# Optimization experiments

Measured on AMD Instinct MI355X. Metric: run time of the kernel, lower is better.

Reference implementation:

```python
import jax, jax.numpy as jnp
import numpy as np

EPS = 1e-8
N = 4
B = 1_000_000


def setup_inputs() -> dict:
    key = jax.random.key(0)
    g = jax.random.normal(key, (B, N, N), dtype=jnp.float32)
    # SPD covariance-like matrices: G G^T + 0.1 I (well-conditioned, distinct eigvals)
    x = jnp.einsum('bik,bjk->bij', g, g) / N + 0.1 * jnp.eye(N, dtype=jnp.float32)
    return {"x": x}


def reference(x):
    # 1) symmetrize + epsilon regularization (ensure SPD)
    sym = 0.5 * (x + jnp.swapaxes(x, -1, -2)) + EPS * jnp.eye(N, dtype=x.dtype)
    # 2) exact matrix log via eigendecomposition
    w, v = jnp.linalg.eigh(sym)                      # w: [B, N], v: [B, N, N]
    log_w = jnp.log(jnp.maximum(w, EPS))
    logm = jnp.einsum('bik,bk,bjk->bij', v, log_w, v)  # V diag(log w) V^T
    # 3) re-symmetrize
    logm = 0.5 * (logm + jnp.swapaxes(logm, -1, -2))
    # 4) upper-triangular vectorization, row-major (i, j>=i) order
    iu, ju = jnp.triu_indices(N)
    return logm[:, iu, ju]                           # [B, N*(N+1)//2]
```

## Files before the change

### kernel.cpp

```cpp
#include <hip/hip_runtime.h>
#include <math.h>

#ifndef NSWEEP
#define NSWEEP 5
#endif

#define EPSV 1e-8f

__device__ __forceinline__ float fast_sqrtf(float x) {
#if __has_builtin(__builtin_amdgcn_sqrtf)
  return __builtin_amdgcn_sqrtf(x);
#else
  return sqrtf(x);
#endif
}
__device__ __forceinline__ float fast_rcpf(float x) {
#if __has_builtin(__builtin_amdgcn_rcpf)
  return __builtin_amdgcn_rcpf(x);
#else
  return 1.0f / x;
#endif
}
__device__ __forceinline__ float fast_rsqf(float x) {
#if __has_builtin(__builtin_amdgcn_rsqf)
  return __builtin_amdgcn_rsqf(x);
#else
  return rsqrtf(x);
#endif
}
__device__ __forceinline__ float fast_logf(float x) {
#if __has_builtin(__builtin_amdgcn_logf)
  return __builtin_amdgcn_logf(x) * 0.6931471805599453f;
#else
  return logf(x);
#endif
}

#define JROT(APP, AQQ, APQ, AK1P, AK1Q, AK2P, AK2Q,                       \
             VP0, VQ0, VP1, VQ1, VP2, VQ2, VP3, VQ3)                      \
  do {                                                                    \
    float a_ = APQ;                                                       \
    float d_ = AQQ - APP;                                                 \
    float a2_ = a_ + a_;                                                  \
    float r_ = fast_sqrtf(fmaf(d_, d_, a2_ * a2_));                       \
    float den_ = fmaxf(fabsf(d_) + r_, 1e-30f);                          \
                        \
    float num_ = __int_as_float(__float_as_int(a2_) ^                     \
                                (__float_as_int(d_) & 0x80000000));       \
    float t_ = num_ * fast_rcpf(den_);                                    \
    float c_ = fast_rsqf(fmaf(t_, t_, 1.0f));                             \
    float s_ = t_ * c_;                                                   \
    float ta_ = t_ * a_;                                                  \
    APP = APP - ta_;                                                      \
    AQQ = AQQ + ta_;                                                      \
    APQ = 0.0f;                                                           \
    {                                                                     \
      float kp_ = AK1P, kq_ = AK1Q;                                       \
      AK1P = fmaf(c_, kp_, -s_ * kq_);                                    \
      AK1Q = fmaf(s_, kp_, c_ * kq_);                                     \
    }                                                                     \
    {                                                                     \
      float kp_ = AK2P, kq_ = AK2Q;                                       \
      AK2P = fmaf(c_, kp_, -s_ * kq_);                                    \
      AK2Q = fmaf(s_, kp_, c_ * kq_);                                     \
    }                                                                     \
    {                                                                     \
      float p_ = VP0, q_ = VQ0;                                           \
      VP0 = fmaf(c_, p_, -s_ * q_);                                       \
      VQ0 = fmaf(s_, p_, c_ * q_);                                        \
    }                                                                     \
    {                                                                     \
      float p_ = VP1, q_ = VQ1;                                           \
      VP1 = fmaf(c_, p_, -s_ * q_);                                       \
      VQ1 = fmaf(s_, p_, c_ * q_);                                        \
    }                                                                     \
    {                                                                     \
      float p_ = VP2, q_ = VQ2;                                           \
      VP2 = fmaf(c_, p_, -s_ * q_);                                       \
      VQ2 = fmaf(s_, p_, c_ * q_);                                        \
    }                                                                     \
    {                                                                     \
      float p_ = VP3, q_ = VQ3;                                           \
      VP3 = fmaf(c_, p_, -s_ * q_);                                       \
      VQ3 = fmaf(s_, p_, c_ * q_);                                        \
    }                                                                     \
  } while (0)

__global__ __launch_bounds__(256) void TangentSpaceLayer_64141041598486_kernel(
    const float* __restrict__ x, float* __restrict__ out, int B) {
  __shared__ __align__(16) float so[256 * 10];
  const int t = threadIdx.x;
  const int m = blockIdx.x * 256 + t;

  if (m < B) {
    const float* p = x + (size_t)m * 16;
    float4 r0 = *(const float4*)(p + 0);
    float4 r1 = *(const float4*)(p + 4);
    float4 r2 = *(const float4*)(p + 8);
    float4 r3 = *(const float4*)(p + 12);

    float a00 = r0.x + EPSV;
    float a01 = 0.5f * (r0.y + r1.x);
    float a02 = 0.5f * (r0.z + r2.x);
    float a03 = 0.5f * (r0.w + r3.x);
    float a11 = r1.y + EPSV;
    float a12 = 0.5f * (r1.z + r2.y);
    float a13 = 0.5f * (r1.w + r3.y);
    float a22 = r2.z + EPSV;
    float a23 = 0.5f * (r2.w + r3.z);
    float a33 = r3.w + EPSV;

    float v00 = 1.f, v01 = 0.f, v02 = 0.f, v03 = 0.f;
    float v10 = 0.f, v11 = 1.f, v12 = 0.f, v13 = 0.f;
    float v20 = 0.f, v21 = 0.f, v22 = 1.f, v23 = 0.f;
    float v30 = 0.f, v31 = 0.f, v32 = 0.f, v33 = 1.f;

#pragma unroll 1
    for (int sweep = 0; sweep < NSWEEP; ++sweep) {
      JROT(a00, a11, a01, a02, a12, a03, a13,
           v00, v01, v10, v11, v20, v21, v30, v31);
      JROT(a00, a22, a02, a01, a12, a03, a23,
           v00, v02, v10, v12, v20, v22, v30, v32);
      JROT(a00, a33, a03, a01, a13, a02, a23,
           v00, v03, v10, v13, v20, v23, v30, v33);
      JROT(a11, a22, a12, a01, a02, a13, a23,
           v01, v02, v11, v12, v21, v22, v31, v32);
      JROT(a11, a33, a13, a01, a03, a12, a23,
           v01, v03, v11, v13, v21, v23, v31, v33);
      JROT(a22, a33, a23, a02, a03, a12, a13,
           v02, v03, v12, v13, v22, v23, v32, v33);
    }

    float lw0 = fast_logf(fmaxf(a00, EPSV));
    float lw1 = fast_logf(fmaxf(a11, EPSV));
    float lw2 = fast_logf(fmaxf(a22, EPSV));
    float lw3 = fast_logf(fmaxf(a33, EPSV));

    float w00 = v00 * lw0, w01 = v01 * lw1, w02 = v02 * lw2, w03 = v03 * lw3;
    float w10 = v10 * lw0, w11 = v11 * lw1, w12 = v12 * lw2, w13 = v13 * lw3;
    float w20 = v20 * lw0, w21 = v21 * lw1, w22 = v22 * lw2, w23 = v23 * lw3;
    float w30 = v30 * lw0, w31 = v31 * lw1, w32 = v32 * lw2, w33 = v33 * lw3;

    float* sp = so + t * 10;
    sp[0] = fmaf(w00, v00, fmaf(w01, v01, fmaf(w02, v02, w03 * v03)));
    sp[1] = fmaf(w00, v10, fmaf(w01, v11, fmaf(w02, v12, w03 * v13)));
    sp[2] = fmaf(w00, v20, fmaf(w01, v21, fmaf(w02, v22, w03 * v23)));
    sp[3] = fmaf(w00, v30, fmaf(w01, v31, fmaf(w02, v32, w03 * v33)));
    sp[4] = fmaf(w10, v10, fmaf(w11, v11, fmaf(w12, v12, w13 * v13)));
    sp[5] = fmaf(w10, v20, fmaf(w11, v21, fmaf(w12, v22, w13 * v23)));
    sp[6] = fmaf(w10, v30, fmaf(w11, v31, fmaf(w12, v32, w13 * v33)));
    sp[7] = fmaf(w20, v20, fmaf(w21, v21, fmaf(w22, v22, w23 * v23)));
    sp[8] = fmaf(w20, v30, fmaf(w21, v31, fmaf(w22, v32, w23 * v33)));
    sp[9] = fmaf(w30, v30, fmaf(w31, v31, fmaf(w32, v32, w33 * v33)));
  }

  __syncthreads();

  const int valid = min(256, B - blockIdx.x * 256);
  const int nf = valid * 10;
  const int n4 = nf >> 2;
  float* obase = out + (size_t)blockIdx.x * 2560;
  const float4* s4 = (const float4*)so;
  float4* o4 = (float4*)obase;
  for (int i = t; i < n4; i += 256) o4[i] = s4[i];
  for (int i = n4 * 4 + t; i < nf; i += 256) obase[i] = so[i];
}

extern "C" void kernel_launch(void* const* d_in, const int* in_sizes, int n_in,
                              void* d_out, int out_size, void* d_ws, size_t ws_size,
                              hipStream_t stream) {
  const float* x = (const float*)d_in[0];
  float* out = (float*)d_out;
  const int B = in_sizes[0] / 16;
  const int blocks = (B + 255) / 256;
  hipLaunchKernelGGL(TangentSpaceLayer_64141041598486_kernel, dim3(blocks),
                     dim3(256), 0, stream, x, out, B);
}
```

Before: 118.3 us.

## Process two matrices per thread and cut Jacobi sweeps to four

Each thread now loads and diagonalizes two 4x4 matrices, with the per-matrix work factored into a device function. Each block covers 512 matrices staged through a larger shared buffer, and the grid is halved. Separately, the cyclic Jacobi sweep count drops from five to four, removing a fifth of the rotation arithmetic at some risk to eigenvalue accuracy for harder inputs. The dual-matrix layout gives more independent work per thread for latency hiding but raises register pressure.

```diff
diff --git a/kernel.cpp b/kernel.cpp
--- a/kernel.cpp
+++ b/kernel.cpp
@@ -2,7 +2,7 @@
 #include <math.h>
 
 #ifndef NSWEEP
-#define NSWEEP 5
+#define NSWEEP 4
 #endif
 
 #define EPSV 1e-8f
@@ -44,7 +44,6 @@
     float a2_ = a_ + a_;                                                  \
     float r_ = fast_sqrtf(fmaf(d_, d_, a2_ * a2_));                       \
     float den_ = fmaxf(fabsf(d_) + r_, 1e-30f);                          \
-                        \
     float num_ = __int_as_float(__float_as_int(a2_) ^                     \
                                 (__float_as_int(d_) & 0x80000000));       \
     float t_ = num_ * fast_rcpf(den_);                                    \
@@ -54,112 +53,118 @@
     APP = APP - ta_;                                                      \
     AQQ = AQQ + ta_;                                                      \
     APQ = 0.0f;                                                           \
-    {                                                                     \
-      float kp_ = AK1P, kq_ = AK1Q;                                       \
+    { float kp_ = AK1P, kq_ = AK1Q;                                       \
       AK1P = fmaf(c_, kp_, -s_ * kq_);                                    \
-      AK1Q = fmaf(s_, kp_, c_ * kq_);                                     \
-    }                                                                     \
-    {                                                                     \
-      float kp_ = AK2P, kq_ = AK2Q;                                       \
+      AK1Q = fmaf(s_, kp_, c_ * kq_); }                                   \
+    { float kp_ = AK2P, kq_ = AK2Q;                                       \
       AK2P = fmaf(c_, kp_, -s_ * kq_);                                    \
-      AK2Q = fmaf(s_, kp_, c_ * kq_);                                     \
-    }                                                                     \
-    {                                                                     \
-      float p_ = VP0, q_ = VQ0;                                           \
+      AK2Q = fmaf(s_, kp_, c_ * kq_); }                                   \
+    { float p_ = VP0, q_ = VQ0;                                           \
       VP0 = fmaf(c_, p_, -s_ * q_);                                       \
-      VQ0 = fmaf(s_, p_, c_ * q_);                                        \
-    }                                                                     \
-    {                                                                     \
-      float p_ = VP1, q_ = VQ1;                                           \
+      VQ0 = fmaf(s_, p_, c_ * q_); }                                      \
+    { float p_ = VP1, q_ = VQ1;                                           \
       VP1 = fmaf(c_, p_, -s_ * q_);                                       \
-      VQ1 = fmaf(s_, p_, c_ * q_);                                        \
-    }                                                                     \
-    {                                                                     \
-      float p_ = VP2, q_ = VQ2;                                           \
+      VQ1 = fmaf(s_, p_, c_ * q_); }                                      \
+    { float p_ = VP2, q_ = VQ2;                                           \
       VP2 = fmaf(c_, p_, -s_ * q_);                                       \
-      VQ2 = fmaf(s_, p_, c_ * q_);                                        \
-    }                                                                     \
-    {                                                                     \
-      float p_ = VP3, q_ = VQ3;                                           \
+      VQ2 = fmaf(s_, p_, c_ * q_); }                                      \
+    { float p_ = VP3, q_ = VQ3;                                           \
       VP3 = fmaf(c_, p_, -s_ * q_);                                       \
-      VQ3 = fmaf(s_, p_, c_ * q_);                                        \
-    }                                                                     \
+      VQ3 = fmaf(s_, p_, c_ * q_); }                                      \
   } while (0)
+
+__device__ __forceinline__ void logm_one(float4 r0, float4 r1, float4 r2,
+                                         float4 r3, float o[10]) {
+  float a00 = r0.x + EPSV;
+  float a01 = 0.5f * (r0.y + r1.x);
+  float a02 = 0.5f * (r0.z + r2.x);
+  float a03 = 0.5f * (r0.w + r3.x);
+  float a11 = r1.y + EPSV;
+  float a12 = 0.5f * (r1.z + r2.y);
+  float a13 = 0.5f * (r1.w + r3.y);
+  float a22 = r2.z + EPSV;
+  float a23 = 0.5f * (r2.w + r3.z);
+  float a33 = r3.w + EPSV;
+
+  float v00 = 1.f, v01 = 0.f, v02 = 0.f, v03 = 0.f;
+  float v10 = 0.f, v11 = 1.f, v12 = 0.f, v13 = 0.f;
+  float v20 = 0.f, v21 = 0.f, v22 = 1.f, v23 = 0.f;
+  float v30 = 0.f, v31 = 0.f, v32 = 0.f, v33 = 1.f;
+
+#pragma unroll 1
+  for (int sweep = 0; sweep < NSWEEP; ++sweep) {
+    JROT(a00, a11, a01, a02, a12, a03, a13,
+         v00, v01, v10, v11, v20, v21, v30, v31);
+    JROT(a00, a22, a02, a01, a12, a03, a23,
+         v00, v02, v10, v12, v20, v22, v30, v32);
+    JROT(a00, a33, a03, a01, a13, a02, a23,
+         v00, v03, v10, v13, v20, v23, v30, v33);
+    JROT(a11, a22, a12, a01, a02, a13, a23,
+         v01, v02, v11, v12, v21, v22, v31, v32);
+    JROT(a11, a33, a13, a01, a03, a12, a23,
+         v01, v03, v11, v13, v21, v23, v31, v33);
+    JROT(a22, a33, a23, a02, a03, a12, a13,
+         v02, v03, v12, v13, v22, v23, v32, v33);
+  }
+
+  float lw0 = fast_logf(fmaxf(a00, EPSV));
+  float lw1 = fast_logf(fmaxf(a11, EPSV));
+  float lw2 = fast_logf(fmaxf(a22, EPSV));
+  float lw3 = fast_logf(fmaxf(a33, EPSV));
+
+  float w00 = v00 * lw0, w01 = v01 * lw1, w02 = v02 * lw2, w03 = v03 * lw3;
+  float w10 = v10 * lw0, w11 = v11 * lw1, w12 = v12 * lw2, w13 = v13 * lw3;
+  float w20 = v20 * lw0, w21 = v21 * lw1, w22 = v22 * lw2, w23 = v23 * lw3;
+  float w30 = v30 * lw0, w31 = v31 * lw1, w32 = v32 * lw2, w33 = v33 * lw3;
+
+  o[0] = fmaf(w00, v00, fmaf(w01, v01, fmaf(w02, v02, w03 * v03)));
+  o[1] = fmaf(w00, v10, fmaf(w01, v11, fmaf(w02, v12, w03 * v13)));
+  o[2] = fmaf(w00, v20, fmaf(w01, v21, fmaf(w02, v22, w03 * v23)));
+  o[3] = fmaf(w00, v30, fmaf(w01, v31, fmaf(w02, v32, w03 * v33)));
+  o[4] = fmaf(w10, v10, fmaf(w11, v11, fmaf(w12, v12, w13 * v13)));
+  o[5] = fmaf(w10, v20, fmaf(w11, v21, fmaf(w12, v22, w13 * v23)));
+  o[6] = fmaf(w10, v30, fmaf(w11, v31, fmaf(w12, v32, w13 * v33)));
+  o[7] = fmaf(w20, v20, fmaf(w21, v21, fmaf(w22, v22, w23 * v23)));
+  o[8] = fmaf(w20, v30, fmaf(w21, v31, fmaf(w22, v32, w23 * v33)));
+  o[9] = fmaf(w30, v30, fmaf(w31, v31, fmaf(w32, v32, w33 * v33)));
+}
 
 __global__ __launch_bounds__(256) void TangentSpaceLayer_64141041598486_kernel(
     const float* __restrict__ x, float* __restrict__ out, int B) {
-  __shared__ __align__(16) float so[256 * 10];
+  __shared__ __align__(16) float so[512 * 10];
   const int t = threadIdx.x;
-  const int m = blockIdx.x * 256 + t;
+  const int base = blockIdx.x * 512;
+  const int m0 = min(base + t, B - 1);
+  const int m1 = min(base + 256 + t, B - 1);
 
-  if (m < B) {
-    const float* p = x + (size_t)m * 16;
-    float4 r0 = *(const float4*)(p + 0);
-    float4 r1 = *(const float4*)(p + 4);
-    float4 r2 = *(const float4*)(p + 8);
-    float4 r3 = *(const float4*)(p + 12);
+  const float* p0 = x + (size_t)m0 * 16;
+  const float* p1 = x + (size_t)m1 * 16;
+  float4 a0 = *(const float4*)(p0 + 0);
+  float4 a1 = *(const float4*)(p0 + 4);
+  float4 a2 = *(const float4*)(p0 + 8);
+  float4 a3 = *(const float4*)(p0 + 12);
+  float4 b0 = *(const float4*)(p1 + 0);
+  float4 b1 = *(const float4*)(p1 + 4);
+  float4 b2 = *(const float4*)(p1 + 8);
+  float4 b3 = *(const float4*)(p1 + 12);
 
-    float a00 = r0.x + EPSV;
-    float a01 = 0.5f * (r0.y + r1.x);
-    float a02 = 0.5f * (r0.z + r2.x);
-    float a03 = 0.5f * (r0.w + r3.x);
-    float a11 = r1.y + EPSV;
-    float a12 = 0.5f * (r1.z + r2.y);
-    float a13 = 0.5f * (r1.w + r3.y);
-    float a22 = r2.z + EPSV;
-    float a23 = 0.5f * (r2.w + r3.z);
-    float a33 = r3.w + EPSV;
+  float oA[10], oB[10];
+  logm_one(a0, a1, a2, a3, oA);
+  logm_one(b0, b1, b2, b3, oB);
 
-    float v00 = 1.f, v01 = 0.f, v02 = 0.f, v03 = 0.f;
-    float v10 = 0.f, v11 = 1.f, v12 = 0.f, v13 = 0.f;
-    float v20 = 0.f, v21 = 0.f, v22 = 1.f, v23 = 0.f;
-    float v30 = 0.f, v31 = 0.f, v32 = 0.f, v33 = 1.f;
-
-#pragma unroll 1
-    for (int sweep = 0; sweep < NSWEEP; ++sweep) {
-      JROT(a00, a11, a01, a02, a12, a03, a13,
-           v00, v01, v10, v11, v20, v21, v30, v31);
-      JROT(a00, a22, a02, a01, a12, a03, a23,
-           v00, v02, v10, v12, v20, v22, v30, v32);
-      JROT(a00, a33, a03, a01, a13, a02, a23,
-           v00, v03, v10, v13, v20, v23, v30, v33);
-      JROT(a11, a22, a12, a01, a02, a13, a23,
-           v01, v02, v11, v12, v21, v22, v31, v32);
-      JROT(a11, a33, a13, a01, a03, a12, a23,
-           v01, v03, v11, v13, v21, v23, v31, v33);
-      JROT(a22, a33, a23, a02, a03, a12, a13,
-           v02, v03, v12, v13, v22, v23, v32, v33);
-    }
-
-    float lw0 = fast_logf(fmaxf(a00, EPSV));
-    float lw1 = fast_logf(fmaxf(a11, EPSV));
-    float lw2 = fast_logf(fmaxf(a22, EPSV));
-    float lw3 = fast_logf(fmaxf(a33, EPSV));
-
-    float w00 = v00 * lw0, w01 = v01 * lw1, w02 = v02 * lw2, w03 = v03 * lw3;
-    float w10 = v10 * lw0, w11 = v11 * lw1, w12 = v12 * lw2, w13 = v13 * lw3;
-    float w20 = v20 * lw0, w21 = v21 * lw1, w22 = v22 * lw2, w23 = v23 * lw3;
-    float w30 = v30 * lw0, w31 = v31 * lw1, w32 = v32 * lw2, w33 = v33 * lw3;
-
-    float* sp = so + t * 10;
-    sp[0] = fmaf(w00, v00, fmaf(w01, v01, fmaf(w02, v02, w03 * v03)));
-    sp[1] = fmaf(w00, v10, fmaf(w01, v11, fmaf(w02, v12, w03 * v13)));
-    sp[2] = fmaf(w00, v20, fmaf(w01, v21, fmaf(w02, v22, w03 * v23)));
-    sp[3] = fmaf(w00, v30, fmaf(w01, v31, fmaf(w02, v32, w03 * v33)));
-    sp[4] = fmaf(w10, v10, fmaf(w11, v11, fmaf(w12, v12, w13 * v13)));
-    sp[5] = fmaf(w10, v20, fmaf(w11, v21, fmaf(w12, v22, w13 * v23)));
-    sp[6] = fmaf(w10, v30, fmaf(w11, v31, fmaf(w12, v32, w13 * v33)));
-    sp[7] = fmaf(w20, v20, fmaf(w21, v21, fmaf(w22, v22, w23 * v23)));
-    sp[8] = fmaf(w20, v30, fmaf(w21, v31, fmaf(w22, v32, w23 * v33)));
-    sp[9] = fmaf(w30, v30, fmaf(w31, v31, fmaf(w32, v32, w33 * v33)));
-  }
+  float* spA = so + t * 10;
+  float* spB = so + (t + 256) * 10;
+#pragma unroll
+  for (int i = 0; i < 10; ++i) spA[i] = oA[i];
+#pragma unroll
+  for (int i = 0; i < 10; ++i) spB[i] = oB[i];
 
   __syncthreads();
 
-  const int valid = min(256, B - blockIdx.x * 256);
+  const int valid = min(512, B - blockIdx.x * 512);
   const int nf = valid * 10;
   const int n4 = nf >> 2;
-  float* obase = out + (size_t)blockIdx.x * 2560;
+  float* obase = out + (size_t)blockIdx.x * 5120;
   const float4* s4 = (const float4*)so;
   float4* o4 = (float4*)obase;
   for (int i = t; i < n4; i += 256) o4[i] = s4[i];
@@ -172,7 +177,7 @@
   const float* x = (const float*)d_in[0];
   float* out = (float*)d_out;
   const int B = in_sizes[0] / 16;
-  const int blocks = (B + 255) / 256;
+  const int blocks = (B + 511) / 512;
   hipLaunchKernelGGL(TangentSpaceLayer_64141041598486_kernel, dim3(blocks),
                      dim3(256), 0, stream, x, out, B);
 }
```

Measured after the change: 113.4 us. 1.04x faster.
